# Kernel tuning notes

Measured on AMD Instinct MI355X. Metric: run time of the kernel, lower is better.

The kernel has to match this reference:

```python
import jax, jax.numpy as jnp
import numpy as np

B, C, H, W = 8, 256, 64, 64
CR = C // 8  # reduced channels = 32


def setup_inputs() -> dict:
    key = jax.random.key(0)
    k1, k2, k3, k4 = jax.random.split(key, 4)
    x = jax.random.normal(k1, (B, C, H, W), dtype=jnp.float32)
    # 1x1 conv weights (bias=False) are plain channel matmuls; scale like kaiming (~1/sqrt(fan_in))
    Wt = jax.random.normal(k2, (3 * CR, C), dtype=jnp.float32) * (1.0 / np.sqrt(C))
    Wo = jax.random.normal(k3, (C, CR), dtype=jnp.float32) * (1.0 / np.sqrt(CR))
    scale = jax.random.normal(k4, (1,), dtype=jnp.float32)
    return {"x": x, "Wt": Wt, "Wo": Wo, "scale": scale}


def reference(x, Wt, Wo, scale):
    b, c, h, w = x.shape
    n = h * w
    # 1x1 conv QKV projection: [B, 3*Cr, H, W]
    t = jnp.einsum('oc,bchw->bohw', Wt, x)
    cr = t.shape[1] // 3
    key = t[:, :cr].reshape(b, cr, n)          # [B, Cr, N]
    query = t[:, cr:2 * cr].reshape(b, cr, n)  # [B, Cr, N]
    value = t[:, 2 * cr:].reshape(b, cr, n)    # [B, Cr, N]
    # scores[b, i, j] = sum_c key[b,c,i] * query[b,c,j]  (key^T @ query)
    scores = jnp.einsum('bci,bcj->bij', key, query)  # [B, N, N]
    # torch Softmax(dim=1): normalize over the key axis i
    weights = jax.nn.softmax(scores, axis=1)
    # output[b, c, j] = sum_i value[b,c,i] * weights[b,i,j]
    out = jnp.einsum('bci,bij->bcj', value, weights)  # [B, Cr, N]
    out = out.reshape(b, cr, h, w)
    out = jnp.einsum('oc,bchw->bohw', Wo, out)  # 1x1 conv back to C channels
    return scale[0] * out + x
```

## Files before the change

### kernel.cpp

```cpp
#include <hip/hip_runtime.h>
#include <math.h>

#define B_ 8
#define C_ 256
#define CR_ 32
#define N_ 4096

typedef __attribute__((ext_vector_type(8))) short bf16x8;
typedef __attribute__((ext_vector_type(4))) short bf16x4;
typedef __attribute__((ext_vector_type(4))) float f32x4;
typedef __attribute__((ext_vector_type(16))) float f32x16;

__device__ inline short f2bf(float f) {
  union { float f; unsigned u; } v; v.f = f;
  unsigned r = v.u + 0x7FFFu + ((v.u >> 16) & 1u);
  return (short)(r >> 16);
}
__device__ inline float bf2f(short h) {
  union { unsigned u; float f; } v; v.u = ((unsigned)(unsigned short)h) << 16;
  return v.f;
}
__device__ inline short f2bf_r(float f) {
  return (short)((__float_as_uint(f) + 0x8000u) >> 16);
}

__global__ __launch_bounds__(256) void prep_weights(const float* __restrict__ Wt,
                                                    const float* __restrict__ Wo,
                                                    const float* __restrict__ scale,
                                                    short* __restrict__ WtHi,
                                                    short* __restrict__ WtLo,
                                                    short* __restrict__ WoB) {
  const int blk = blockIdx.x, tid = threadIdx.x;
  if (blk < 96) {
    float v = Wt[blk * C_ + tid];
    if (blk >= 32 && blk < 64) v *= 1.44269504f;
    const short h = f2bf(v);
    WtHi[blk * C_ + tid] = h;
    WtLo[blk * C_ + tid] = f2bf(v - bf2f(h));
  } else {
    const int idx = (blk - 96) * 256 + tid;
    WoB[idx] = f2bf(Wo[idx] * scale[0]);
  }
}

__global__ __launch_bounds__(256) void qkv_mfma(const float* __restrict__ x,
                                                const short* __restrict__ WtHi,
                                                const short* __restrict__ WtLo,
                                                short* __restrict__ t_tr,
                                                short* __restrict__ Vg) {
  const int b = blockIdx.y;
  const int tid = threadIdx.x;
  const int wave = tid >> 6, lane = tid & 63;
  const int col = lane & 15, quad = lane >> 4;
  const int n0 = (blockIdx.x * 4 + wave) * 16;

  const f32x4 z4 = {0.f, 0.f, 0.f, 0.f};
  f32x4 acc[6] = {z4, z4, z4, z4, z4, z4};

  const float* xb = x + (size_t)b * C_ * N_ + n0 + col;
  float xcur[8], xnxt[8];
#pragma unroll
  for (int j = 0; j < 8; ++j) xcur[j] = xb[(size_t)(quad * 8 + j) * N_];

#pragma unroll 2
  for (int c0 = 0; c0 < C_; c0 += 32) {
    if (c0 < C_ - 32) {
#pragma unroll
      for (int j = 0; j < 8; ++j)
        xnxt[j] = xb[(size_t)(c0 + 32 + quad * 8 + j) * N_];
    }
    bf16x8 xh, xl;
#pragma unroll
    for (int j = 0; j < 8; ++j) {
      const short h = (short)(__float_as_uint(xcur[j]) >> 16);
      xh[j] = h;
      xl[j] = f2bf_r(xcur[j] - bf2f(h));
    }
#pragma unroll
    for (int ot = 0; ot < 4; ++ot) {
      const int off = (ot * 16 + col) * C_ + c0 + quad * 8;
      const bf16x8 bh = *(const bf16x8*)(WtHi + off);
      const bf16x8 bl = *(const bf16x8*)(WtLo + off);
      acc[ot] = __builtin_amdgcn_mfma_f32_16x16x32_bf16(xh, bh, acc[ot], 0, 0, 0);
      acc[ot] = __builtin_amdgcn_mfma_f32_16x16x32_bf16(xl, bh, acc[ot], 0, 0, 0);
      acc[ot] = __builtin_amdgcn_mfma_f32_16x16x32_bf16(xh, bl, acc[ot], 0, 0, 0);
    }
#pragma unroll
    for (int ct = 0; ct < 2; ++ct) {
      const int off = ((64 + ct * 16) + col) * C_ + c0 + quad * 8;
      const bf16x8 ah = *(const bf16x8*)(WtHi + off);
      const bf16x8 al = *(const bf16x8*)(WtLo + off);
      acc[4 + ct] = __builtin_amdgcn_mfma_f32_16x16x32_bf16(ah, xh, acc[4 + ct], 0, 0, 0);
      acc[4 + ct] = __builtin_amdgcn_mfma_f32_16x16x32_bf16(ah, xl, acc[4 + ct], 0, 0, 0);
      acc[4 + ct] = __builtin_amdgcn_mfma_f32_16x16x32_bf16(al, xh, acc[4 + ct], 0, 0, 0);
    }
#pragma unroll
    for (int j = 0; j < 8; ++j) xcur[j] = xnxt[j];
  }
#pragma unroll
  for (int ot = 0; ot < 4; ++ot)
#pragma unroll
    for (int r = 0; r < 4; ++r)
      t_tr[((size_t)b * N_ + n0 + quad * 4 + r) * 64 + ot * 16 + col] =
          f2bf(acc[ot][r]);
#pragma unroll
  for (int ct = 0; ct < 2; ++ct)
#pragma unroll
    for (int r = 0; r < 4; ++r)
      Vg[(size_t)b * CR_ * N_ + (size_t)(ct * 16 + quad * 4 + r) * N_ + n0 + col] =
          f2bf(acc[4 + ct][r]);
}

__global__ __launch_bounds__(64, 2) void flash_attn(const short* __restrict__ t_tr,
                                                    const short* __restrict__ Vg,
                                                    short* __restrict__ OPart,
                                                    float* __restrict__ LPart) {
  const int b = blockIdx.z, hq = blockIdx.y;
  const int j0 = blockIdx.x * 64;
  const int lane = threadIdx.x;
  const int j32 = lane & 31, h32 = lane >> 5;
  const short* T = t_tr + (size_t)b * N_ * 64;
  const short* V = Vg + (size_t)b * CR_ * N_;

  const f32x16 z16 = {0.f};
  bf16x8 qf[2][2];
#pragma unroll
  for (int jt = 0; jt < 2; ++jt)
#pragma unroll
    for (int ch = 0; ch < 2; ++ch)
      qf[jt][ch] = *(const bf16x8*)(T + (size_t)(j0 + jt * 32 + j32) * 64 + 32 +
                                    ch * 16 + h32 * 8);

  f32x16 acc[2] = {z16, z16};
  float ps[2] = {0.f, 0.f};

  const int ibase = hq * 1024;
  bf16x8 kf[4], vf[4], kfn[4], vfn[4];
#pragma unroll
  for (int it = 0; it < 2; ++it)
#pragma unroll
    for (int ch = 0; ch < 2; ++ch)
      kf[it * 2 + ch] = *(const bf16x8*)(T + (size_t)(ibase + it * 32 + j32) * 64 +
                                         ch * 16 + h32 * 8);
#pragma unroll
  for (int ich = 0; ich < 4; ++ich)
    vf[ich] = *(const bf16x8*)(V + (size_t)j32 * N_ + ibase + ich * 16 + h32 * 8);

  for (int iter = 0; iter < 16; ++iter) {
    const int inx = ibase + ((iter + 1) & 15) * 64;
#pragma unroll
    for (int it = 0; it < 2; ++it)
#pragma unroll
      for (int ch = 0; ch < 2; ++ch)
        kfn[it * 2 + ch] = *(const bf16x8*)(T + (size_t)(inx + it * 32 + j32) * 64 +
                                            ch * 16 + h32 * 8);
#pragma unroll
    for (int ich = 0; ich < 4; ++ich)
      vfn[ich] = *(const bf16x8*)(V + (size_t)j32 * N_ + inx + ich * 16 + h32 * 8);

#pragma unroll
    for (int it = 0; it < 2; ++it) {
#pragma unroll
      for (int jt = 0; jt < 2; ++jt) {
        f32x16 s = __builtin_amdgcn_mfma_f32_32x32x16_bf16(kf[it * 2 + 0], qf[jt][0], z16, 0, 0, 0);
        s = __builtin_amdgcn_mfma_f32_32x32x16_bf16(kf[it * 2 + 1], qf[jt][1], s, 0, 0, 0);
        float p[16];
#pragma unroll
        for (int r = 0; r < 16; ++r) p[r] = __builtin_amdgcn_exp2f(s[r]);
        ps[jt] += (((p[0] + p[1]) + (p[2] + p[3])) + ((p[4] + p[5]) + (p[6] + p[7]))) +
                  (((p[8] + p[9]) + (p[10] + p[11])) + ((p[12] + p[13]) + (p[14] + p[15])));
        unsigned d[8], xw[8];
#pragma unroll
        for (int k = 0; k < 8; ++k) {
          const unsigned u0 = __float_as_uint(p[2 * k]) + 0x8000u;
          const unsigned u1 = __float_as_uint(p[2 * k + 1]) + 0x8000u;
          d[k] = __builtin_amdgcn_perm(u1, u0, 0x07060302u);
        }
#pragma unroll
        for (int k = 0; k < 8; ++k) xw[k] = __shfl_xor((int)d[k], 32);
        union { unsigned u[4]; bf16x8 v; } f0, f1;
        f0.u[0] = h32 ? xw[2] : d[0];
        f0.u[1] = h32 ? xw[3] : d[1];
        f0.u[2] = h32 ? d[2] : xw[0];
        f0.u[3] = h32 ? d[3] : xw[1];
        f1.u[0] = h32 ? xw[6] : d[4];
        f1.u[1] = h32 ? xw[7] : d[5];
        f1.u[2] = h32 ? d[6] : xw[4];
        f1.u[3] = h32 ? d[7] : xw[5];
        acc[jt] = __builtin_amdgcn_mfma_f32_32x32x16_bf16(vf[it * 2 + 0], f0.v, acc[jt], 0, 0, 0);
        acc[jt] = __builtin_amdgcn_mfma_f32_32x32x16_bf16(vf[it * 2 + 1], f1.v, acc[jt], 0, 0, 0);
      }
    }
#pragma unroll
    for (int k = 0; k < 4; ++k) { kf[k] = kfn[k]; vf[k] = vfn[k]; }
  }

  const size_t base = ((size_t)b * 4 + hq) * N_;
#pragma unroll
  for (int jt = 0; jt < 2; ++jt) {
    const float l = ps[jt] + __shfl_xor(ps[jt], 32);
    const int jg = j0 + jt * 32 + j32;
    if (h32 == 0) LPart[base + jg] = l;
    short* OP = OPart + (base + jg) * 32;
#pragma unroll
    for (int g = 0; g < 4; ++g) {
      bf16x4 o = {f2bf(acc[jt][4 * g + 0]), f2bf(acc[jt][4 * g + 1]),
                  f2bf(acc[jt][4 * g + 2]), f2bf(acc[jt][4 * g + 3])};
      *(bf16x4*)(OP + 8 * g + 4 * h32) = o;
    }
  }
}

__global__ __launch_bounds__(256) void out_proj(const short* __restrict__ OPart,
                                                const float* __restrict__ LPart,
                                                const short* __restrict__ WoB,
                                                const float* __restrict__ x,
                                                float* __restrict__ out) {
  const int b = blockIdx.z, chalf = blockIdx.y;
  const int tid = threadIdx.x;
  const int wave = tid >> 6, lane = tid & 63;
  const int col = lane & 15, quad = lane >> 4;
  const int jg = blockIdx.x * 64 + wave * 16 + col;
  const int n0 = blockIdx.x * 64 + wave * 16;

  float osum[8];
#pragma unroll
  for (int e = 0; e < 8; ++e) osum[e] = 0.f;
  float lsum = 0.f;
#pragma unroll
  for (int h = 0; h < 4; ++h) {
    const size_t p = ((size_t)b * 4 + h) * N_ + jg;
    const bf16x8 o = *(const bf16x8*)(OPart + p * 32 + quad * 8);
#pragma unroll
    for (int e = 0; e < 8; ++e) osum[e] += bf2f(o[e]);
    lsum += LPart[p];
  }
  const float linv = 1.f / lsum;
  bf16x8 bf;
#pragma unroll
  for (int e = 0; e < 8; ++e) bf[e] = f2bf(osum[e] * linv);

  const f32x4 z4 = {0.f, 0.f, 0.f, 0.f};
  const float* xb = x + (size_t)b * C_ * N_;
  float* ob = out + (size_t)b * C_ * N_;
#pragma unroll
  for (int ct = 0; ct < 8; ++ct) {
    const int ctg = chalf * 8 + ct;
    const bf16x8 af = *(const bf16x8*)(WoB + (ctg * 16 + col) * 32 + quad * 8);
    const f32x4 a = __builtin_amdgcn_mfma_f32_16x16x32_bf16(af, bf, z4, 0, 0, 0);
#pragma unroll
    for (int r = 0; r < 4; ++r) {
      const size_t idx = (size_t)(ctg * 16 + quad * 4 + r) * N_ + n0 + col;
      ob[idx] = a[r] + xb[idx];
    }
  }
}

extern "C" void kernel_launch(void* const* d_in, const int* in_sizes, int n_in,
                              void* d_out, int out_size, void* d_ws,
                              size_t ws_size, hipStream_t stream) {
  const float* x = (const float*)d_in[0];
  const float* Wt = (const float*)d_in[1];
  const float* Wo = (const float*)d_in[2];
  const float* scale = (const float*)d_in[3];
  float* out = (float*)d_out;

  short* OPart = (short*)d_ws;
  float* LPart = (float*)(OPart + (size_t)B_ * 4 * N_ * 32);
  short* t_tr = (short*)(LPart + (size_t)B_ * 4 * N_);
  short* Vg = t_tr + (size_t)B_ * N_ * 64;
  short* WtHi = Vg + (size_t)B_ * CR_ * N_;
  short* WtLo = WtHi + 96 * C_;
  short* WoB = WtLo + 96 * C_;

  prep_weights<<<dim3(128), 256, 0, stream>>>(Wt, Wo, scale, WtHi, WtLo, WoB);
  qkv_mfma<<<dim3(64, B_), 256, 0, stream>>>(x, WtHi, WtLo, t_tr, Vg);
  flash_attn<<<dim3(64, 4, B_), 64, 0, stream>>>(t_tr, Vg, OPart, LPart);
  out_proj<<<dim3(64, 2, B_), 256, 0, stream>>>(OPart, LPart, WoB, x, out);
}
```

Before: 157.5 us.

## Split QKV channel reduction across waves, raise attention key split, vectorize output

The QKV projection now splits the 256-channel reduction between two waves per column tile, combines the partial sums through shared memory, and doubles the grid to 128 blocks per batch. Flash attention splits keys eight ways instead of four and drops V prefetch double-buffering to save registers, raising the occupancy hint to 3. The output projection stages MFMA results through LDS so the residual x reads and output writes become float4 coalesced accesses. The larger key split doubles the partial-output traffic and the per-element reduction work in out_proj.

Result: no change. 158.6 us (+0.7%).

```diff
diff --git a/kernel.cpp b/kernel.cpp
--- a/kernel.cpp
+++ b/kernel.cpp
@@ -5,6 +5,7 @@
 #define C_ 256
 #define CR_ 32
 #define N_ 4096
+#define KSPLIT 8
 
 typedef __attribute__((ext_vector_type(8))) short bf16x8;
 typedef __attribute__((ext_vector_type(4))) short bf16x4;
@@ -51,8 +52,12 @@
   const int b = blockIdx.y;
   const int tid = threadIdx.x;
   const int wave = tid >> 6, lane = tid & 63;
+  const int pair = wave >> 1, chalf = wave & 1;
   const int col = lane & 15, quad = lane >> 4;
-  const int n0 = (blockIdx.x * 4 + wave) * 16;
+  const int n0 = (blockIdx.x * 2 + pair) * 16;
+  const int cbase = chalf * 128;
+
+  __shared__ float Ms[2][64][25];
 
   const f32x4 z4 = {0.f, 0.f, 0.f, 0.f};
   f32x4 acc[6] = {z4, z4, z4, z4, z4, z4};
@@ -60,11 +65,11 @@
   const float* xb = x + (size_t)b * C_ * N_ + n0 + col;
   float xcur[8], xnxt[8];
 #pragma unroll
-  for (int j = 0; j < 8; ++j) xcur[j] = xb[(size_t)(quad * 8 + j) * N_];
-
-#pragma unroll 2
-  for (int c0 = 0; c0 < C_; c0 += 32) {
-    if (c0 < C_ - 32) {
+  for (int j = 0; j < 8; ++j) xcur[j] = xb[(size_t)(cbase + quad * 8 + j) * N_];
+
+#pragma unroll
+  for (int c0 = cbase; c0 < cbase + 128; c0 += 32) {
+    if (c0 < cbase + 96) {
 #pragma unroll
       for (int j = 0; j < 8; ++j)
         xnxt[j] = xb[(size_t)(c0 + 32 + quad * 8 + j) * N_];
@@ -97,21 +102,37 @@
 #pragma unroll
     for (int j = 0; j < 8; ++j) xcur[j] = xnxt[j];
   }
-#pragma unroll
-  for (int ot = 0; ot < 4; ++ot)
-#pragma unroll
-    for (int r = 0; r < 4; ++r)
-      t_tr[((size_t)b * N_ + n0 + quad * 4 + r) * 64 + ot * 16 + col] =
-          f2bf(acc[ot][r]);
-#pragma unroll
-  for (int ct = 0; ct < 2; ++ct)
-#pragma unroll
-    for (int r = 0; r < 4; ++r)
-      Vg[(size_t)b * CR_ * N_ + (size_t)(ct * 16 + quad * 4 + r) * N_ + n0 + col] =
-          f2bf(acc[4 + ct][r]);
-}
-
-__global__ __launch_bounds__(64, 2) void flash_attn(const short* __restrict__ t_tr,
+
+  if (chalf) {
+    float* dst = &Ms[pair][lane][0];
+#pragma unroll
+    for (int t = 0; t < 6; ++t)
+#pragma unroll
+      for (int r = 0; r < 4; ++r) dst[t * 4 + r] = acc[t][r];
+  }
+  __syncthreads();
+  if (!chalf) {
+    const float* src = &Ms[pair][lane][0];
+#pragma unroll
+    for (int t = 0; t < 6; ++t)
+#pragma unroll
+      for (int r = 0; r < 4; ++r) acc[t][r] += src[t * 4 + r];
+#pragma unroll
+    for (int ot = 0; ot < 4; ++ot)
+#pragma unroll
+      for (int r = 0; r < 4; ++r)
+        t_tr[((size_t)b * N_ + n0 + quad * 4 + r) * 64 + ot * 16 + col] =
+            f2bf(acc[ot][r]);
+#pragma unroll
+    for (int ct = 0; ct < 2; ++ct)
+#pragma unroll
+      for (int r = 0; r < 4; ++r)
+        Vg[(size_t)b * CR_ * N_ + (size_t)(ct * 16 + quad * 4 + r) * N_ + n0 + col] =
+            f2bf(acc[4 + ct][r]);
+  }
+}
+
+__global__ __launch_bounds__(64, 3) void flash_attn(const short* __restrict__ t_tr,
                                                     const short* __restrict__ Vg,
                                                     short* __restrict__ OPart,
                                                     float* __restrict__ LPart) {
@@ -134,29 +155,28 @@
   f32x16 acc[2] = {z16, z16};
   float ps[2] = {0.f, 0.f};
 
-  const int ibase = hq * 1024;
-  bf16x8 kf[4], vf[4], kfn[4], vfn[4];
+  const int ibase = hq * (N_ / KSPLIT);
+  int i0 = ibase;
+  bf16x8 kf[4], kfn[4];
 #pragma unroll
   for (int it = 0; it < 2; ++it)
 #pragma unroll
     for (int ch = 0; ch < 2; ++ch)
       kf[it * 2 + ch] = *(const bf16x8*)(T + (size_t)(ibase + it * 32 + j32) * 64 +
                                          ch * 16 + h32 * 8);
-#pragma unroll
-  for (int ich = 0; ich < 4; ++ich)
-    vf[ich] = *(const bf16x8*)(V + (size_t)j32 * N_ + ibase + ich * 16 + h32 * 8);
-
-  for (int iter = 0; iter < 16; ++iter) {
-    const int inx = ibase + ((iter + 1) & 15) * 64;
+
+  for (int iter = 0; iter < 8; ++iter) {
+    const int inx = ibase + ((iter + 1) & 7) * 64;
+    bf16x8 vf[4];
+#pragma unroll
+    for (int ich = 0; ich < 4; ++ich)
+      vf[ich] = *(const bf16x8*)(V + (size_t)j32 * N_ + i0 + ich * 16 + h32 * 8);
 #pragma unroll
     for (int it = 0; it < 2; ++it)
 #pragma unroll
       for (int ch = 0; ch < 2; ++ch)
         kfn[it * 2 + ch] = *(const bf16x8*)(T + (size_t)(inx + it * 32 + j32) * 64 +
                                             ch * 16 + h32 * 8);
-#pragma unroll
-    for (int ich = 0; ich < 4; ++ich)
-      vfn[ich] = *(const bf16x8*)(V + (size_t)j32 * N_ + inx + ich * 16 + h32 * 8);
 
 #pragma unroll
     for (int it = 0; it < 2; ++it) {
@@ -191,11 +211,12 @@
         acc[jt] = __builtin_amdgcn_mfma_f32_32x32x16_bf16(vf[it * 2 + 1], f1.v, acc[jt], 0, 0, 0);
       }
     }
-#pragma unroll
-    for (int k = 0; k < 4; ++k) { kf[k] = kfn[k]; vf[k] = vfn[k]; }
-  }
-
-  const size_t base = ((size_t)b * 4 + hq) * N_;
+    i0 = inx;
+#pragma unroll
+    for (int k = 0; k < 4; ++k) kf[k] = kfn[k];
+  }
+
+  const size_t base = ((size_t)b * KSPLIT + hq) * N_;
 #pragma unroll
   for (int jt = 0; jt < 2; ++jt) {
     const float l = ps[jt] + __shfl_xor(ps[jt], 32);
@@ -220,16 +241,19 @@
   const int tid = threadIdx.x;
   const int wave = tid >> 6, lane = tid & 63;
   const int col = lane & 15, quad = lane >> 4;
-  const int jg = blockIdx.x * 64 + wave * 16 + col;
   const int n0 = blockIdx.x * 64 + wave * 16;
+  const int jg = n0 + col;
+  const int coL = lane >> 2, n4 = lane & 3;
+
+  __shared__ float Ls[4][2][16][20];
 
   float osum[8];
 #pragma unroll
   for (int e = 0; e < 8; ++e) osum[e] = 0.f;
   float lsum = 0.f;
 #pragma unroll
-  for (int h = 0; h < 4; ++h) {
-    const size_t p = ((size_t)b * 4 + h) * N_ + jg;
+  for (int h = 0; h < KSPLIT; ++h) {
+    const size_t p = ((size_t)b * KSPLIT + h) * N_ + jg;
     const bf16x8 o = *(const bf16x8*)(OPart + p * 32 + quad * 8);
 #pragma unroll
     for (int e = 0; e < 8; ++e) osum[e] += bf2f(o[e]);
@@ -240,19 +264,31 @@
 #pragma unroll
   for (int e = 0; e < 8; ++e) bf[e] = f2bf(osum[e] * linv);
 
-  const f32x4 z4 = {0.f, 0.f, 0.f, 0.f};
   const float* xb = x + (size_t)b * C_ * N_;
   float* ob = out + (size_t)b * C_ * N_;
+  float4 xv[8];
+#pragma unroll
+  for (int ct = 0; ct < 8; ++ct) {
+    const int ctg = chalf * 8 + ct;
+    xv[ct] = *(const float4*)(xb + (size_t)(ctg * 16 + coL) * N_ + n0 + n4 * 4);
+  }
+
+  const f32x4 z4 = {0.f, 0.f, 0.f, 0.f};
 #pragma unroll
   for (int ct = 0; ct < 8; ++ct) {
     const int ctg = chalf * 8 + ct;
     const bf16x8 af = *(const bf16x8*)(WoB + (ctg * 16 + col) * 32 + quad * 8);
     const f32x4 a = __builtin_amdgcn_mfma_f32_16x16x32_bf16(af, bf, z4, 0, 0, 0);
-#pragma unroll
-    for (int r = 0; r < 4; ++r) {
-      const size_t idx = (size_t)(ctg * 16 + quad * 4 + r) * N_ + n0 + col;
-      ob[idx] = a[r] + xb[idx];
-    }
+    float* L = &Ls[wave][ct & 1][0][0];
+#pragma unroll
+    for (int r = 0; r < 4; ++r) L[(quad * 4 + r) * 20 + col] = a[r];
+    const float4 lv = *(const float4*)&Ls[wave][ct & 1][coL][n4 * 4];
+    float4 o;
+    o.x = lv.x + xv[ct].x;
+    o.y = lv.y + xv[ct].y;
+    o.z = lv.z + xv[ct].z;
+    o.w = lv.w + xv[ct].w;
+    *(float4*)(ob + (size_t)(ctg * 16 + coL) * N_ + n0 + n4 * 4) = o;
   }
 }
 
@@ -266,15 +302,15 @@
   float* out = (float*)d_out;
 
   short* OPart = (short*)d_ws;
-  float* LPart = (float*)(OPart + (size_t)B_ * 4 * N_ * 32);
-  short* t_tr = (short*)(LPart + (size_t)B_ * 4 * N_);
+  float* LPart = (float*)(OPart + (size_t)B_ * KSPLIT * N_ * 32);
+  short* t_tr = (short*)(LPart + (size_t)B_ * KSPLIT * N_);
   short* Vg = t_tr + (size_t)B_ * N_ * 64;
   short* WtHi = Vg + (size_t)B_ * CR_ * N_;
   short* WtLo = WtHi + 96 * C_;
   short* WoB = WtLo + 96 * C_;
 
   prep_weights<<<dim3(128), 256, 0, stream>>>(Wt, Wo, scale, WtHi, WtLo, WoB);
-  qkv_mfma<<<dim3(64, B_), 256, 0, stream>>>(x, WtHi, WtLo, t_tr, Vg);
-  flash_attn<<<dim3(64, 4, B_), 64, 0, stream>>>(t_tr, Vg, OPart, LPart);
+  qkv_mfma<<<dim3(128, B_), 256, 0, stream>>>(x, WtHi, WtLo, t_tr, Vg);
+  flash_attn<<<dim3(64, KSPLIT, B_), 64, 0, stream>>>(t_tr, Vg, OPart, LPart);
   out_proj<<<dim3(64, 2, B_), 256, 0, stream>>>(OPart, LPart, WoB, x, out);
 }
```
